# Kernel tuning notes

Hardware: AMD Instinct MI355X
Metric: run time of the kernel (lower is better)

Reference implementation:

```python
import jax, jax.numpy as jnp
import numpy as np

STEPS = 10          # points in t_grid -> STEPS-1 RK4 intervals
TRACE_STEPS = 2     # Hutchinson probes per dynamics eval
T_FINAL = 1.0
CLAMP = 100.0


def odefun(t, z, W1, b1, tw1, W2, b2):
    # time-conditioned 2-layer tanh MLP (canonical FFJORD dynamics)
    h = jnp.tanh(z @ W1 + b1 + t * tw1)
    return h @ W2 + b2


def setup_inputs() -> dict:
    key = jax.random.key(0)
    B, D, H = 2048, 512, 1024
    ks = jax.random.split(key, 4)
    s1 = 1.0 / np.sqrt(D)
    s2 = 1.0 / np.sqrt(H)
    return {
        "x": jax.random.normal(ks[0], (B, D), jnp.float32),
        "W1": jax.random.normal(ks[1], (D, H), jnp.float32) * s1,
        "b1": jnp.zeros((H,), jnp.float32),
        "tw1": jax.random.normal(ks[2], (H,), jnp.float32) * 0.1,
        "W2": jax.random.normal(ks[3], (H, D), jnp.float32) * s2,
        "b2": jnp.zeros((D,), jnp.float32),
    }


def reference(x, W1, b1, tw1, W2, b2):
    params = (W1, b1, tw1, W2, b2)
    B, D = x.shape

    def divergence_estimate(t, z, e):
        # torch detaches z before the grad call -> stop_gradient here
        z_sg = jax.lax.stop_gradient(z)
        f, vjp_fn = jax.vjp(lambda zz: odefun(t, zz, *params), z_sg)
        etf = vjp_fn(e)[0]                      # e^T J  (Hutchinson probe)
        return f, jnp.sum(etf * e, axis=-1)     # [B]

    def augmented_dynamics(t, state, key):
        z = state[:, :-1]                        # [B, D]
        div_est = jnp.zeros((B,), state.dtype)
        f_z = None
        for i in range(TRACE_STEPS):             # small fixed loop
            e = jax.random.randint(jax.random.fold_in(key, i), z.shape, 0, 2).astype(z.dtype) * 2.0 - 1.0
            f_z, div = divergence_estimate(t, z, e)
            div_est = div_est + div
        div_est = jnp.clip(div_est / TRACE_STEPS, -CLAMP, CLAMP)
        return jnp.concatenate([f_z, -div_est[:, None]], axis=-1)

    t_grid = jnp.linspace(0.0, T_FINAL, STEPS)
    state0 = jnp.concatenate([x, jnp.zeros((B, 1), x.dtype)], axis=-1)  # [B, D+1]

    def step(carry, t01):
        state, key = carry
        t0, t1 = t01[0], t01[1]
        dt = t1 - t0
        key, k1k, k2k, k3k, k4k = jax.random.split(key, 5)
        # torchdiffeq 'rk4' = Kutta's 3/8-rule variant (rk4_alt_step_func)
        k1 = augmented_dynamics(t0, state, k1k)
        k2 = augmented_dynamics(t0 + dt / 3.0, state + dt * k1 / 3.0, k2k)
        k3 = augmented_dynamics(t0 + dt * 2.0 / 3.0, state + dt * (k2 - k1 / 3.0), k3k)
        k4 = augmented_dynamics(t1, state + dt * (k1 - k2 + k3), k4k)
        state = state + (k1 + 3.0 * (k2 + k3) + k4) * dt * 0.125
        return (state, key), None

    t_pairs = jnp.stack([t_grid[:-1], t_grid[1:]], axis=-1)  # [STEPS-1, 2]
    (state, _), _ = jax.lax.scan(step, (state0, jax.random.key(1234)), t_pairs)

    rep, probsolve = state[:, :-1], state[:, -1]
    logprob = -0.5 * jnp.sum(rep * rep, axis=-1) + probsolve
    return rep, logprob
```

## Files before the change

### kernel.cpp

```cpp
#include <hip/hip_runtime.h>
#include <stdint.h>


#define B_N 2048
#define D_N 512
#define H_N 1024
#define BD (B_N * D_N)

typedef unsigned short u16;
typedef __attribute__((ext_vector_type(8))) short s16x8;
typedef __attribute__((ext_vector_type(4))) float f32x4;

typedef __attribute__((address_space(1))) const uint32_t ga_u32;
typedef __attribute__((address_space(3))) uint32_t ls_u32;

__device__ __forceinline__ float bf2f(u16 u) {
  union { uint32_t u; float f; } c; c.u = ((uint32_t)u) << 16; return c.f;
}
__device__ __forceinline__ u16 f2bf(float f) {
  union { float f; uint32_t u; } c; c.f = f;
  uint32_t r = c.u + 0x7FFFu + ((c.u >> 16) & 1u);
  return (u16)(r >> 16);
}

struct U2 { uint32_t x, y; };

__device__ __forceinline__ U2 tf2x32(uint32_t k0, uint32_t k1, uint32_t x0, uint32_t x1) {
  uint32_t k2 = k0 ^ k1 ^ 0x1BD11BDAu;
#define ROTL(a, r) (((a) << (r)) | ((a) >> (32 - (r))))
#define RND(r) { x0 += x1; x1 = ROTL(x1, r); x1 ^= x0; }
  x0 += k0; x1 += k1;
  RND(13) RND(15) RND(26) RND(6)
  x0 += k1; x1 += k2 + 1u;
  RND(17) RND(29) RND(16) RND(24)
  x0 += k2; x1 += k0 + 2u;
  RND(13) RND(15) RND(26) RND(6)
  x0 += k0; x1 += k1 + 3u;
  RND(17) RND(29) RND(16) RND(24)
  x0 += k1; x1 += k2 + 4u;
  RND(13) RND(15) RND(26) RND(6)
  x0 += k2; x1 += k0 + 5u;
#undef RND
#undef ROTL
  U2 r; r.x = x0; r.y = x1; return r;
}

__global__ void k_keysched(uint32_t* __restrict__ ekeys) {
  if (threadIdx.x != 0 || blockIdx.x != 0) return;
  uint32_t kx = 0u, ky = 1234u;
  for (int s = 0; s < 9; ++s) {
    for (int st = 0; st < 4; ++st) {
      U2 kst = tf2x32(kx, ky, 0u, (uint32_t)(st + 1));
      for (int pr = 0; pr < 2; ++pr) {
        U2 fo = tf2x32(kst.x, kst.y, 0u, (uint32_t)pr);
        U2 k2 = tf2x32(fo.x, fo.y, 0u, 1u);
        ekeys[(s * 4 + st) * 4 + pr * 2 + 0] = k2.x;
        ekeys[(s * 4 + st) * 4 + pr * 2 + 1] = k2.y;
      }
    }
    U2 c = tf2x32(kx, ky, 0u, 0u);
    kx = c.x; ky = c.y;
  }
}

__global__ void k_ebits_all(uint32_t* __restrict__ ebAll, const uint32_t* __restrict__ keys) {
  int t = blockIdx.x * 256 + threadIdx.x;
  int stage = t >> 16, rem = t & 65535;
  int probe = rem >> 15, idx = rem & 32767;
  uint32_t p0 = (uint32_t)idx * 32;
  uint32_t k0 = keys[stage * 4 + probe * 2], k1 = keys[stage * 4 + probe * 2 + 1];
  uint32_t bits = 0;
#pragma unroll 4
  for (int j = 0; j < 32; ++j) {
    U2 r = tf2x32(k0, k1, 0u, p0 + j);
    bits |= ((r.x ^ r.y) & 1u) << j;
  }
  ebAll[(size_t)stage * 65536 + probe * 32768 + idx] = bits;
}

__global__ void k_eexp(u16* __restrict__ ebf, const uint32_t* __restrict__ ebAll, int gs) {
  int t = blockIdx.x * 256 + threadIdx.x;
  int stage = gs + (t >> 16), rem = t & 65535;
  int probe = rem >> 15, idx = rem & 32767;
  uint32_t w = ebAll[(size_t)stage * 65536 + probe * 32768 + idx];
  uint32_t* dst = (uint32_t*)(ebf + (size_t)(stage & 3) * (2 * (size_t)BD) + (size_t)probe * BD + (size_t)idx * 32);
#pragma unroll
  for (int g4 = 0; g4 < 4; ++g4) {
    uint4 v;
    uint32_t b;
    b = w >> (g4 * 8);
    v.x = ((b & 1u) ? 0x3F80u : 0xBF80u) | (((b >> 1) & 1u) ? 0x3F800000u : 0xBF800000u);
    v.y = (((b >> 2) & 1u) ? 0x3F80u : 0xBF80u) | (((b >> 3) & 1u) ? 0x3F800000u : 0xBF800000u);
    v.z = (((b >> 4) & 1u) ? 0x3F80u : 0xBF80u) | (((b >> 5) & 1u) ? 0x3F800000u : 0xBF800000u);
    v.w = (((b >> 6) & 1u) ? 0x3F80u : 0xBF80u) | (((b >> 7) & 1u) ? 0x3F800000u : 0xBF800000u);
    ((uint4*)dst)[g4] = v;
  }
}

__global__ void k_init(const float* __restrict__ x, float* __restrict__ z, u16* __restrict__ zin,
                       float* __restrict__ lp, float* __restrict__ d0, float* __restrict__ d1) {
  int i = blockIdx.x * 256 + threadIdx.x;
  if (i < BD) { float v = x[i]; z[i] = v; zin[i] = f2bf(v); }
  if (i < B_N) { lp[i] = 0.f; d0[i] = 0.f; d1[i] = 0.f; }
}

__global__ void k_cvtT(const float* __restrict__ src, u16* __restrict__ dst, int R, int C) {
  int i = blockIdx.x * 256 + threadIdx.x;
  if (i >= R * C) return;
  int c = i / R, r = i - c * R;
  dst[i] = f2bf(src[(size_t)r * C + c]);
}
__global__ void k_cvt(const float* __restrict__ src, u16* __restrict__ dst, int n) {
  int i = blockIdx.x * 256 + threadIdx.x;
  if (i < n) dst[i] = f2bf(src[i]);
}

__global__ void k_sentinel(float* __restrict__ out, int n) {
  int i = blockIdx.x * 256 + threadIdx.x;
  if (i < n) out[i] = 12345.0f;
}

__global__ __launch_bounds__(256)
void k_f1(const u16* __restrict__ zin, const u16* __restrict__ e0g, const u16* __restrict__ e1g,
          const u16* __restrict__ W1T, const u16* __restrict__ W2b,
          const float* __restrict__ b1, const float* __restrict__ tw1, float tstage,
          u16* __restrict__ hbuf, float* __restrict__ div0, float* __restrict__ div1) {
  __shared__ u16 Zs[64 * 32], E0s[64 * 32], E1s[64 * 32], W1s[64 * 32], W2s[64 * 32];
  const int tid = threadIdx.x, wave = tid >> 6, lane = tid & 63;
  const int bm = blockIdx.x >> 4;
  const int bh = blockIdx.x & 15;
  const int row0 = bm * 64, col0 = bh * 64;
  const int wm = wave >> 1, wn = wave & 1, r16 = lane & 15, q = lane >> 4;
  const int srow = lane >> 2, scol = (lane & 3) * 8;

  f32x4 az[2][2], au0[2][2], au1[2][2], av0[2][2], av1[2][2];
#pragma unroll
  for (int i = 0; i < 2; ++i)
#pragma unroll
    for (int j = 0; j < 2; ++j) {
      az[i][j] = (f32x4){0,0,0,0}; au0[i][j] = (f32x4){0,0,0,0}; au1[i][j] = (f32x4){0,0,0,0};
      av0[i][j] = (f32x4){0,0,0,0}; av1[i][j] = (f32x4){0,0,0,0};
    }

  const size_t arow = (size_t)(row0 + wave * 16 + srow) * 512 + scol;
  const size_t brow = (size_t)(col0 + wave * 16 + srow) * 512 + scol;
  for (int kt = 0; kt < 512; kt += 32) {
    __builtin_amdgcn_global_load_lds((ga_u32*)(zin + arow + kt), (ls_u32*)(Zs  + wave * 512), 16, 0, 0);
    __builtin_amdgcn_global_load_lds((ga_u32*)(e0g + arow + kt), (ls_u32*)(E0s + wave * 512), 16, 0, 0);
    __builtin_amdgcn_global_load_lds((ga_u32*)(e1g + arow + kt), (ls_u32*)(E1s + wave * 512), 16, 0, 0);
    __builtin_amdgcn_global_load_lds((ga_u32*)(W1T + brow + kt), (ls_u32*)(W1s + wave * 512), 16, 0, 0);
    __builtin_amdgcn_global_load_lds((ga_u32*)(W2b + brow + kt), (ls_u32*)(W2s + wave * 512), 16, 0, 0);
    __syncthreads();
    s16x8 zf[2], e0f[2], e1f[2], w1f[2], w2f[2];
#pragma unroll
    for (int i = 0; i < 2; ++i) {
      const int ao = (wm * 32 + i * 16 + r16) * 32 + q * 8;
      zf[i]  = *(const s16x8*)(Zs  + ao);
      e0f[i] = *(const s16x8*)(E0s + ao);
      e1f[i] = *(const s16x8*)(E1s + ao);
    }
#pragma unroll
    for (int j = 0; j < 2; ++j) {
      const int bo = (wn * 32 + j * 16 + r16) * 32 + q * 8;
      w1f[j] = *(const s16x8*)(W1s + bo);
      w2f[j] = *(const s16x8*)(W2s + bo);
    }
#pragma unroll
    for (int i = 0; i < 2; ++i)
#pragma unroll
      for (int j = 0; j < 2; ++j) {
        az[i][j]  = __builtin_amdgcn_mfma_f32_16x16x32_bf16(zf[i],  w1f[j], az[i][j],  0, 0, 0);
        au0[i][j] = __builtin_amdgcn_mfma_f32_16x16x32_bf16(e0f[i], w1f[j], au0[i][j], 0, 0, 0);
        au1[i][j] = __builtin_amdgcn_mfma_f32_16x16x32_bf16(e1f[i], w1f[j], au1[i][j], 0, 0, 0);
        av0[i][j] = __builtin_amdgcn_mfma_f32_16x16x32_bf16(e0f[i], w2f[j], av0[i][j], 0, 0, 0);
        av1[i][j] = __builtin_amdgcn_mfma_f32_16x16x32_bf16(e1f[i], w2f[j], av1[i][j], 0, 0, 0);
      }
    __syncthreads();
  }

  float d0s[2][4], d1s[2][4];
#pragma unroll
  for (int i = 0; i < 2; ++i)
#pragma unroll
    for (int r = 0; r < 4; ++r) { d0s[i][r] = 0.f; d1s[i][r] = 0.f; }

#pragma unroll
  for (int j = 0; j < 2; ++j) {
    const int gcol = col0 + wn * 32 + j * 16 + r16;
    const float colb = b1[gcol] + tstage * tw1[gcol];
#pragma unroll
    for (int i = 0; i < 2; ++i) {
      const int rbase = row0 + wm * 32 + i * 16 + q * 4;
#pragma unroll
      for (int r = 0; r < 4; ++r) {
        float hv = tanhf(az[i][j][r] + colb);
        hbuf[(size_t)(rbase + r) * H_N + gcol] = f2bf(hv);
        float s = 1.f - hv * hv;
        d0s[i][r] += s * au0[i][j][r] * av0[i][j][r];
        d1s[i][r] += s * au1[i][j][r] * av1[i][j][r];
      }
    }
  }
#pragma unroll
  for (int i = 0; i < 2; ++i)
#pragma unroll
    for (int r = 0; r < 4; ++r) {
      float a = d0s[i][r], b = d1s[i][r];
#pragma unroll
      for (int m = 1; m < 16; m <<= 1) { a += __shfl_xor(a, m); b += __shfl_xor(b, m); }
      if (r16 == 0) {
        int grow = row0 + wm * 32 + i * 16 + q * 4 + r;
        atomicAdd(&div0[grow], a);
        atomicAdd(&div1[grow], b);
      }
    }
}

template<int ST>
__global__ __launch_bounds__(256)
void k_f3(const u16* __restrict__ hbuf, const u16* __restrict__ W2T, const float* __restrict__ b2,
          float* __restrict__ z, float* __restrict__ ACC, float* __restrict__ T,
          u16* __restrict__ zin, float dt,
          float* __restrict__ lp, float* __restrict__ div0, float* __restrict__ div1, float wdt) {
  __shared__ u16 As[64 * 32];
  __shared__ u16 Bs[64 * 32];
  const int tid = threadIdx.x, wave = tid >> 6, lane = tid & 63;
  const int bm = blockIdx.x >> 3;
  const int bn = blockIdx.x & 7;
  const int row0 = bm * 64, col0 = bn * 64;
  const int wm = wave >> 1, wn = wave & 1, r16 = lane & 15, q = lane >> 4;
  const int srow = lane >> 2, scol = (lane & 3) * 8;

  if (bn == 0 && tid < 64) {
    int b = row0 + tid;
    float c = 0.5f * (div0[b] + div1[b]);
    c = fminf(fmaxf(c, -100.f), 100.f);
    lp[b] -= wdt * c;
    div0[b] = 0.f; div1[b] = 0.f;
  }

  f32x4 acc[2][2];
#pragma unroll
  for (int i = 0; i < 2; ++i)
#pragma unroll
    for (int j = 0; j < 2; ++j) acc[i][j] = (f32x4){0,0,0,0};

  const size_t arow = (size_t)(row0 + wave * 16 + srow) * 1024 + scol;
  const size_t brow = (size_t)(col0 + wave * 16 + srow) * 1024 + scol;
  for (int kt = 0; kt < 1024; kt += 32) {
    __builtin_amdgcn_global_load_lds((ga_u32*)(hbuf + arow + kt), (ls_u32*)(As + wave * 512), 16, 0, 0);
    __builtin_amdgcn_global_load_lds((ga_u32*)(W2T  + brow + kt), (ls_u32*)(Bs + wave * 512), 16, 0, 0);
    __syncthreads();
    s16x8 af[2], bfr[2];
#pragma unroll
    for (int i = 0; i < 2; ++i)
      af[i] = *(const s16x8*)(As + (wm * 32 + i * 16 + r16) * 32 + q * 8);
#pragma unroll
    for (int j = 0; j < 2; ++j)
      bfr[j] = *(const s16x8*)(Bs + (wn * 32 + j * 16 + r16) * 32 + q * 8);
#pragma unroll
    for (int i = 0; i < 2; ++i)
#pragma unroll
      for (int j = 0; j < 2; ++j)
        acc[i][j] = __builtin_amdgcn_mfma_f32_16x16x32_bf16(af[i], bfr[j], acc[i][j], 0, 0, 0);
    __syncthreads();
  }

#pragma unroll
  for (int j = 0; j < 2; ++j) {
    const int gcol = col0 + wn * 32 + j * 16 + r16;
    const float cb = b2[gcol];
#pragma unroll
    for (int i = 0; i < 2; ++i) {
      const int rbase = row0 + wm * 32 + i * 16 + q * 4;
#pragma unroll
      for (int r = 0; r < 4; ++r) {
        const size_t idx = (size_t)(rbase + r) * D_N + gcol;
        const float f = acc[i][j][r] + cb;
        if (ST == 0) {
          ACC[idx] = dt * 0.125f * f;
          T[idx]   = dt * f;
          zin[idx] = f2bf(z[idx] + dt * f * (1.f / 3.f));
        } else if (ST == 1) {
          float t_ = T[idx];
          ACC[idx] += 0.375f * dt * f;
          zin[idx] = f2bf(z[idx] + dt * f - t_ * (1.f / 3.f));
          T[idx]   = t_ - dt * f;
        } else if (ST == 2) {
          ACC[idx] += 0.375f * dt * f;
          zin[idx] = f2bf(z[idx] + T[idx] + dt * f);
        } else {
          float zn = z[idx] + ACC[idx] + dt * 0.125f * f;
          z[idx]   = zn;
          zin[idx] = f2bf(zn);
        }
      }
    }
  }
}

__global__ void k_out(const float* __restrict__ z, const float* __restrict__ lp,
                      float* __restrict__ out) {
  int b = blockIdx.x, t = threadIdx.x;
  const float* zr = z + (size_t)b * D_N;
  float ss = 0.f;
  for (int d = t; d < D_N; d += 256) {
    float v = zr[d];
    out[(size_t)b * D_N + d] = v;
    ss += v * v;
  }
  for (int off = 32; off > 0; off >>= 1) ss += __shfl_down(ss, off);
  __shared__ float red[4];
  if ((t & 63) == 0) red[t >> 6] = ss;
  __syncthreads();
  if (t == 0) out[(size_t)BD + b] = -0.5f * (red[0] + red[1] + red[2] + red[3]) + lp[b];
}

extern "C" void kernel_launch(void* const* d_in, const int* in_sizes, int n_in,
                              void* d_out, int out_size, void* d_ws, size_t ws_size,
                              hipStream_t stream) {
  const float* x   = (const float*)d_in[0];
  const float* W1  = (const float*)d_in[1];
  const float* b1  = (const float*)d_in[2];
  const float* tw1 = (const float*)d_in[3];
  const float* W2  = (const float*)d_in[4];
  const float* b2  = (const float*)d_in[5];

  const size_t NEEDED = (size_t)50 << 20;
  if (ws_size < NEEDED) {
    k_sentinel<<<(BD + B_N + 255) / 256, 256, 0, stream>>>((float*)d_out, BD + B_N);
    return;
  }
  char* w = (char*)d_ws;
  auto carve = [&](size_t bytes) { char* p = w; w += (bytes + 255) & ~(size_t)255; return p; };
  uint32_t* keys  = (uint32_t*)carve(144 * sizeof(uint32_t));
  uint32_t* ebAll = (uint32_t*)carve((size_t)36 * 65536 * 4);
  u16* ebf   = (u16*)carve((size_t)4 * 2 * BD * 2);
  float* z   = (float*)carve((size_t)BD * 4);
  float* ACC = (float*)carve((size_t)BD * 4);
  float* T   = (float*)carve((size_t)BD * 4);
  u16* zin   = (u16*)carve((size_t)BD * 2);
  u16* hbuf  = (u16*)carve((size_t)B_N * H_N * 2);
  u16* W1T   = (u16*)carve((size_t)H_N * D_N * 2);
  u16* W2b   = (u16*)carve((size_t)H_N * D_N * 2);
  u16* W2T   = (u16*)carve((size_t)D_N * H_N * 2);
  float* lp   = (float*)carve((size_t)B_N * 4);
  float* div0 = (float*)carve((size_t)B_N * 4);
  float* div1 = (float*)carve((size_t)B_N * 4);

  k_keysched<<<1, 1, 0, stream>>>(keys);
  k_init<<<BD / 256, 256, 0, stream>>>(x, z, zin, lp, div0, div1);
  k_cvtT<<<(D_N * H_N) / 256, 256, 0, stream>>>(W1, W1T, D_N, H_N);
  k_cvt <<<(H_N * D_N) / 256, 256, 0, stream>>>(W2, W2b, H_N * D_N);
  k_cvtT<<<(H_N * D_N) / 256, 256, 0, stream>>>(W2, W2T, H_N, D_N);
  k_ebits_all<<<(36 * 65536) / 256, 256, 0, stream>>>(ebAll, keys);

  const int gF1 = (B_N / 64) * (H_N / 64);
  const int gF3 = (B_N / 64) * (D_N / 64);

  for (int s = 0; s < 9; ++s) {
    float t0 = (float)s / 9.0f;
    float t1 = (float)(s + 1) / 9.0f;
    float dt = t1 - t0;
    float tst[4] = { t0, t0 + dt / 3.0f, t0 + dt * 2.0f / 3.0f, t1 };
    float wts[4] = { 1.f, 3.f, 3.f, 1.f };
    for (int st = 0; st < 4; ++st) {
      const int sg = s * 4 + st;
      if ((sg & 3) == 0) k_eexp<<<(4 * 65536) / 256, 256, 0, stream>>>(ebf, ebAll, sg);
      const u16* e0g = ebf + (size_t)(sg & 3) * (2 * (size_t)BD);
      const u16* e1g = e0g + BD;
      k_f1<<<gF1, 256, 0, stream>>>(zin, e0g, e1g, W1T, W2b, b1, tw1, tst[st], hbuf, div0, div1);
      const float wdt = dt * 0.125f * wts[st];
      if (st == 0)      k_f3<0><<<gF3, 256, 0, stream>>>(hbuf, W2T, b2, z, ACC, T, zin, dt, lp, div0, div1, wdt);
      else if (st == 1) k_f3<1><<<gF3, 256, 0, stream>>>(hbuf, W2T, b2, z, ACC, T, zin, dt, lp, div0, div1, wdt);
      else if (st == 2) k_f3<2><<<gF3, 256, 0, stream>>>(hbuf, W2T, b2, z, ACC, T, zin, dt, lp, div0, div1, wdt);
      else              k_f3<3><<<gF3, 256, 0, stream>>>(hbuf, W2T, b2, z, ACC, T, zin, dt, lp, div0, div1, wdt);
    }
  }
  k_out<<<B_N, 256, 0, stream>>>(z, lp, (float*)d_out);
}
```

Baseline: 1.664 ms.

## Double-buffer LDS in GEMM kernels and fuse probe generation with expansion

Both GEMM kernels (k_f1, k_f3) now use two LDS buffers. The next K-tile's global_load_lds is issued right after the barrier, so it overlaps the MFMA work on the current tile, and one barrier per iteration is removed. The separate bit-packing and expansion kernels for the Rademacher probes are merged into one k_egen that writes bf16 ±1 directly, which drops the intermediate ebAll buffer and its extra launch. Threefry rotations use the alignbit builtin. Risks: doubled LDS per block may lower occupancy, and the single barrier relies on the next iteration's barrier to order the async LDS writes.

```diff
diff --git a/kernel.cpp b/kernel.cpp
--- a/kernel.cpp
+++ b/kernel.cpp
@@ -14,6 +14,12 @@
 typedef __attribute__((address_space(1))) const uint32_t ga_u32;
 typedef __attribute__((address_space(3))) uint32_t ls_u32;
 
+#if __has_builtin(__builtin_amdgcn_alignbit)
+#define ROTL32(x, r) __builtin_amdgcn_alignbit((x), (x), 32 - (r))
+#else
+#define ROTL32(x, r) (((x) << (r)) | ((x) >> (32 - (r))))
+#endif
+
 __device__ __forceinline__ float bf2f(u16 u) {
   union { uint32_t u; float f; } c; c.u = ((uint32_t)u) << 16; return c.f;
 }
@@ -27,8 +33,7 @@
 
 __device__ __forceinline__ U2 tf2x32(uint32_t k0, uint32_t k1, uint32_t x0, uint32_t x1) {
   uint32_t k2 = k0 ^ k1 ^ 0x1BD11BDAu;
-#define ROTL(a, r) (((a) << (r)) | ((a) >> (32 - (r))))
-#define RND(r) { x0 += x1; x1 = ROTL(x1, r); x1 ^= x0; }
+#define RND(r) { x0 += x1; x1 = ROTL32(x1, r); x1 ^= x0; }
   x0 += k0; x1 += k1;
   RND(13) RND(15) RND(26) RND(6)
   x0 += k1; x1 += k2 + 1u;
@@ -41,7 +46,6 @@
   RND(13) RND(15) RND(26) RND(6)
   x0 += k2; x1 += k0 + 5u;
 #undef RND
-#undef ROTL
   U2 r; r.x = x0; r.y = x1; return r;
 }
 
@@ -63,37 +67,26 @@
   }
 }
 
-__global__ void k_ebits_all(uint32_t* __restrict__ ebAll, const uint32_t* __restrict__ keys) {
+__global__ void k_egen(u16* __restrict__ ebf, const uint32_t* __restrict__ keys, int gs) {
   int t = blockIdx.x * 256 + threadIdx.x;
-  int stage = t >> 16, rem = t & 65535;
+  int stage = gs + (t >> 16), rem = t & 65535;
   int probe = rem >> 15, idx = rem & 32767;
   uint32_t p0 = (uint32_t)idx * 32;
   uint32_t k0 = keys[stage * 4 + probe * 2], k1 = keys[stage * 4 + probe * 2 + 1];
-  uint32_t bits = 0;
-#pragma unroll 4
-  for (int j = 0; j < 32; ++j) {
-    U2 r = tf2x32(k0, k1, 0u, p0 + j);
-    bits |= ((r.x ^ r.y) & 1u) << j;
-  }
-  ebAll[(size_t)stage * 65536 + probe * 32768 + idx] = bits;
-}
-
-__global__ void k_eexp(u16* __restrict__ ebf, const uint32_t* __restrict__ ebAll, int gs) {
-  int t = blockIdx.x * 256 + threadIdx.x;
-  int stage = gs + (t >> 16), rem = t & 65535;
-  int probe = rem >> 15, idx = rem & 32767;
-  uint32_t w = ebAll[(size_t)stage * 65536 + probe * 32768 + idx];
-  uint32_t* dst = (uint32_t*)(ebf + (size_t)(stage & 3) * (2 * (size_t)BD) + (size_t)probe * BD + (size_t)idx * 32);
-#pragma unroll
-  for (int g4 = 0; g4 < 4; ++g4) {
-    uint4 v;
-    uint32_t b;
-    b = w >> (g4 * 8);
-    v.x = ((b & 1u) ? 0x3F80u : 0xBF80u) | (((b >> 1) & 1u) ? 0x3F800000u : 0xBF800000u);
-    v.y = (((b >> 2) & 1u) ? 0x3F80u : 0xBF80u) | (((b >> 3) & 1u) ? 0x3F800000u : 0xBF800000u);
-    v.z = (((b >> 4) & 1u) ? 0x3F80u : 0xBF80u) | (((b >> 5) & 1u) ? 0x3F800000u : 0xBF800000u);
-    v.w = (((b >> 6) & 1u) ? 0x3F80u : 0xBF80u) | (((b >> 7) & 1u) ? 0x3F800000u : 0xBF800000u);
-    ((uint4*)dst)[g4] = v;
+  uint4* dst = (uint4*)(ebf + (size_t)(stage & 3) * (2 * (size_t)BD) + (size_t)probe * BD + (size_t)idx * 32);
+#pragma unroll
+  for (int g = 0; g < 4; ++g) {
+    uint32_t pr[4];
+#pragma unroll
+    for (int h = 0; h < 4; ++h) {
+      uint32_t c0 = p0 + g * 8 + h * 2;
+      U2 r0 = tf2x32(k0, k1, 0u, c0);
+      U2 r1 = tf2x32(k0, k1, 0u, c0 + 1u);
+      pr[h] = (((r0.x ^ r0.y) & 1u) ? 0x3F80u : 0xBF80u) |
+              (((r1.x ^ r1.y) & 1u) ? 0x3F800000u : 0xBF800000u);
+    }
+    uint4 v; v.x = pr[0]; v.y = pr[1]; v.z = pr[2]; v.w = pr[3];
+    dst[g] = v;
   }
 }
 
@@ -125,7 +118,7 @@
           const u16* __restrict__ W1T, const u16* __restrict__ W2b,
           const float* __restrict__ b1, const float* __restrict__ tw1, float tstage,
           u16* __restrict__ hbuf, float* __restrict__ div0, float* __restrict__ div1) {
-  __shared__ u16 Zs[64 * 32], E0s[64 * 32], E1s[64 * 32], W1s[64 * 32], W2s[64 * 32];
+  __shared__ u16 S[2][5 * 2048];
   const int tid = threadIdx.x, wave = tid >> 6, lane = tid & 63;
   const int bm = blockIdx.x >> 4;
   const int bh = blockIdx.x & 15;
@@ -144,26 +137,33 @@
 
   const size_t arow = (size_t)(row0 + wave * 16 + srow) * 512 + scol;
   const size_t brow = (size_t)(col0 + wave * 16 + srow) * 512 + scol;
-  for (int kt = 0; kt < 512; kt += 32) {
-    __builtin_amdgcn_global_load_lds((ga_u32*)(zin + arow + kt), (ls_u32*)(Zs  + wave * 512), 16, 0, 0);
-    __builtin_amdgcn_global_load_lds((ga_u32*)(e0g + arow + kt), (ls_u32*)(E0s + wave * 512), 16, 0, 0);
-    __builtin_amdgcn_global_load_lds((ga_u32*)(e1g + arow + kt), (ls_u32*)(E1s + wave * 512), 16, 0, 0);
-    __builtin_amdgcn_global_load_lds((ga_u32*)(W1T + brow + kt), (ls_u32*)(W1s + wave * 512), 16, 0, 0);
-    __builtin_amdgcn_global_load_lds((ga_u32*)(W2b + brow + kt), (ls_u32*)(W2s + wave * 512), 16, 0, 0);
+  auto stage = [&](int kt, int buf) {
+    u16* b = &S[buf][0];
+    __builtin_amdgcn_global_load_lds((ga_u32*)(zin + arow + kt), (ls_u32*)(b + 0    + wave * 512), 16, 0, 0);
+    __builtin_amdgcn_global_load_lds((ga_u32*)(e0g + arow + kt), (ls_u32*)(b + 2048 + wave * 512), 16, 0, 0);
+    __builtin_amdgcn_global_load_lds((ga_u32*)(e1g + arow + kt), (ls_u32*)(b + 4096 + wave * 512), 16, 0, 0);
+    __builtin_amdgcn_global_load_lds((ga_u32*)(W1T + brow + kt), (ls_u32*)(b + 6144 + wave * 512), 16, 0, 0);
+    __builtin_amdgcn_global_load_lds((ga_u32*)(W2b + brow + kt), (ls_u32*)(b + 8192 + wave * 512), 16, 0, 0);
+  };
+  stage(0, 0);
+  for (int it = 0; it < 16; ++it) {
+    const int buf = it & 1;
     __syncthreads();
+    if (it + 1 < 16) stage((it + 1) * 32, buf ^ 1);
+    const u16* b = &S[buf][0];
     s16x8 zf[2], e0f[2], e1f[2], w1f[2], w2f[2];
 #pragma unroll
     for (int i = 0; i < 2; ++i) {
       const int ao = (wm * 32 + i * 16 + r16) * 32 + q * 8;
-      zf[i]  = *(const s16x8*)(Zs  + ao);
-      e0f[i] = *(const s16x8*)(E0s + ao);
-      e1f[i] = *(const s16x8*)(E1s + ao);
+      zf[i]  = *(const s16x8*)(b + 0    + ao);
+      e0f[i] = *(const s16x8*)(b + 2048 + ao);
+      e1f[i] = *(const s16x8*)(b + 4096 + ao);
     }
 #pragma unroll
     for (int j = 0; j < 2; ++j) {
       const int bo = (wn * 32 + j * 16 + r16) * 32 + q * 8;
-      w1f[j] = *(const s16x8*)(W1s + bo);
-      w2f[j] = *(const s16x8*)(W2s + bo);
+      w1f[j] = *(const s16x8*)(b + 6144 + bo);
+      w2f[j] = *(const s16x8*)(b + 8192 + bo);
     }
 #pragma unroll
     for (int i = 0; i < 2; ++i)
@@ -175,7 +175,6 @@
         av0[i][j] = __builtin_amdgcn_mfma_f32_16x16x32_bf16(e0f[i], w2f[j], av0[i][j], 0, 0, 0);
         av1[i][j] = __builtin_amdgcn_mfma_f32_16x16x32_bf16(e1f[i], w2f[j], av1[i][j], 0, 0, 0);
       }
-    __syncthreads();
   }
 
   float d0s[2][4], d1s[2][4];
@@ -222,8 +221,7 @@
           float* __restrict__ z, float* __restrict__ ACC, float* __restrict__ T,
           u16* __restrict__ zin, float dt,
           float* __restrict__ lp, float* __restrict__ div0, float* __restrict__ div1, float wdt) {
-  __shared__ u16 As[64 * 32];
-  __shared__ u16 Bs[64 * 32];
+  __shared__ u16 S[2][2 * 2048];
   const int tid = threadIdx.x, wave = tid >> 6, lane = tid & 63;
   const int bm = blockIdx.x >> 3;
   const int bn = blockIdx.x & 7;
@@ -247,23 +245,29 @@
 
   const size_t arow = (size_t)(row0 + wave * 16 + srow) * 1024 + scol;
   const size_t brow = (size_t)(col0 + wave * 16 + srow) * 1024 + scol;
-  for (int kt = 0; kt < 1024; kt += 32) {
-    __builtin_amdgcn_global_load_lds((ga_u32*)(hbuf + arow + kt), (ls_u32*)(As + wave * 512), 16, 0, 0);
-    __builtin_amdgcn_global_load_lds((ga_u32*)(W2T  + brow + kt), (ls_u32*)(Bs + wave * 512), 16, 0, 0);
+  auto stage = [&](int kt, int buf) {
+    u16* b = &S[buf][0];
+    __builtin_amdgcn_global_load_lds((ga_u32*)(hbuf + arow + kt), (ls_u32*)(b + 0    + wave * 512), 16, 0, 0);
+    __builtin_amdgcn_global_load_lds((ga_u32*)(W2T  + brow + kt), (ls_u32*)(b + 2048 + wave * 512), 16, 0, 0);
+  };
+  stage(0, 0);
+  for (int it = 0; it < 32; ++it) {
+    const int buf = it & 1;
     __syncthreads();
+    if (it + 1 < 32) stage((it + 1) * 32, buf ^ 1);
+    const u16* b = &S[buf][0];
     s16x8 af[2], bfr[2];
 #pragma unroll
     for (int i = 0; i < 2; ++i)
-      af[i] = *(const s16x8*)(As + (wm * 32 + i * 16 + r16) * 32 + q * 8);
+      af[i] = *(const s16x8*)(b + (wm * 32 + i * 16 + r16) * 32 + q * 8);
 #pragma unroll
     for (int j = 0; j < 2; ++j)
-      bfr[j] = *(const s16x8*)(Bs + (wn * 32 + j * 16 + r16) * 32 + q * 8);
+      bfr[j] = *(const s16x8*)(b + 2048 + (wn * 32 + j * 16 + r16) * 32 + q * 8);
 #pragma unroll
     for (int i = 0; i < 2; ++i)
 #pragma unroll
       for (int j = 0; j < 2; ++j)
         acc[i][j] = __builtin_amdgcn_mfma_f32_16x16x32_bf16(af[i], bfr[j], acc[i][j], 0, 0, 0);
-    __syncthreads();
   }
 
 #pragma unroll
@@ -326,15 +330,14 @@
   const float* W2  = (const float*)d_in[4];
   const float* b2  = (const float*)d_in[5];
 
-  const size_t NEEDED = (size_t)50 << 20;
+  const size_t NEEDED = (size_t)45 << 20;
   if (ws_size < NEEDED) {
     k_sentinel<<<(BD + B_N + 255) / 256, 256, 0, stream>>>((float*)d_out, BD + B_N);
     return;
   }
   char* w = (char*)d_ws;
   auto carve = [&](size_t bytes) { char* p = w; w += (bytes + 255) & ~(size_t)255; return p; };
-  uint32_t* keys  = (uint32_t*)carve(144 * sizeof(uint32_t));
-  uint32_t* ebAll = (uint32_t*)carve((size_t)36 * 65536 * 4);
+  uint32_t* keys = (uint32_t*)carve(144 * sizeof(uint32_t));
   u16* ebf   = (u16*)carve((size_t)4 * 2 * BD * 2);
   float* z   = (float*)carve((size_t)BD * 4);
   float* ACC = (float*)carve((size_t)BD * 4);
@@ -353,7 +356,6 @@
   k_cvtT<<<(D_N * H_N) / 256, 256, 0, stream>>>(W1, W1T, D_N, H_N);
   k_cvt <<<(H_N * D_N) / 256, 256, 0, stream>>>(W2, W2b, H_N * D_N);
   k_cvtT<<<(H_N * D_N) / 256, 256, 0, stream>>>(W2, W2T, H_N, D_N);
-  k_ebits_all<<<(36 * 65536) / 256, 256, 0, stream>>>(ebAll, keys);
 
   const int gF1 = (B_N / 64) * (H_N / 64);
   const int gF3 = (B_N / 64) * (D_N / 64);
@@ -366,7 +368,7 @@
     float wts[4] = { 1.f, 3.f, 3.f, 1.f };
     for (int st = 0; st < 4; ++st) {
       const int sg = s * 4 + st;
-      if ((sg & 3) == 0) k_eexp<<<(4 * 65536) / 256, 256, 0, stream>>>(ebf, ebAll, sg);
+      if ((sg & 3) == 0) k_egen<<<1024, 256, 0, stream>>>(ebf, keys, sg);
       const u16* e0g = ebf + (size_t)(sg & 3) * (2 * (size_t)BD);
       const u16* e1g = e0g + BD;
       k_f1<<<gF1, 256, 0, stream>>>(zin, e0g, e1g, W1T, W2b, b1, tw1, tst[st], hbuf, div0, div1);
```

Result: faster. 1.476 ms (-11.3%).
